# Kernel tuning notes

Hardware: AMD Instinct MI355X
Metric: run time of the kernel (lower is better)

Reference implementation:

```python
import jax, jax.numpy as jnp
import numpy as np

N = 500000       # total points
V = 60000        # number of voxels (segments)
XYZ_NORM = jnp.array([20.0, 20.0, 4.0], dtype=jnp.float32)
LN_EPS = 1e-3


def _ln(x, g, b):
    m = jnp.mean(x, axis=-1, keepdims=True)
    v = jnp.var(x, axis=-1, keepdims=True)
    return (x - m) * jax.lax.rsqrt(v + LN_EPS) * g + b


def _mlp_layer(x, w, b, g, be):
    # Linear -> LayerNorm -> ReLU (build_mlp in SST)
    return jax.nn.relu(_ln(x @ w + b, g, be))


def setup_inputs() -> dict:
    key = jax.random.key(0)
    ks = jax.random.split(key, 16)
    d = {
        "points": jax.random.normal(ks[0], (N, 4), jnp.float32) * 10.0,
        "features": jax.random.normal(ks[1], (N, 125), jnp.float32),
        "coors": jax.random.randint(ks[2], (N,), 0, V, jnp.int32),
        "f_cluster": jax.random.normal(ks[3], (N, 3), jnp.float32),
        "w1": jax.random.normal(ks[4], (128, 128), jnp.float32) * 0.05,
        "b1": jnp.zeros((128,), jnp.float32),
        "g1": jnp.ones((128,), jnp.float32),
        "be1": jnp.zeros((128,), jnp.float32),
        "w2": jax.random.normal(ks[5], (128, 256), jnp.float32) * 0.05,
        "b2": jnp.zeros((256,), jnp.float32),
        "g2": jnp.ones((256,), jnp.float32),
        "be2": jnp.zeros((256,), jnp.float32),
        "pw1": jax.random.normal(ks[6], (256, 256), jnp.float32) * 0.05,
        "pb1": jnp.zeros((256,), jnp.float32),
        "pg1": jnp.ones((256,), jnp.float32),
        "pbe1": jnp.zeros((256,), jnp.float32),
        "pw2": jax.random.normal(ks[7], (256, 256), jnp.float32) * 0.05,
        "pb2": jnp.zeros((256,), jnp.float32),
        "pg2": jnp.ones((256,), jnp.float32),
        "pbe2": jnp.zeros((256,), jnp.float32),
        "ow": jax.random.normal(ks[8], (256, 64), jnp.float32) * 0.05,
        "ob": jnp.zeros((64,), jnp.float32),
        "og": jnp.ones((64,), jnp.float32),
        "obe": jnp.zeros((64,), jnp.float32),
    }
    return d


def reference(points, features, coors, f_cluster,
              w1, b1, g1, be1, w2, b2, g2, be2,
              pw1, pb1, pg1, pbe1, pw2, pb2, pg2, pbe2,
              ow, ob, og, obe):
    fc = f_cluster / XYZ_NORM[None, :]
    x = jnp.concatenate([features, fc], axis=1)           # [N, 128]
    x = _mlp_layer(x, w1, b1, g1, be1)                     # [N, 128]
    x = _mlp_layer(x, w2, b2, g2, be2)                     # [N, 256]

    out_pts_feats = _mlp_layer(x, ow, ob, og, obe)         # [N, 64]

    counts = jax.ops.segment_sum(jnp.ones((x.shape[0],), x.dtype), coors,
                                 num_segments=V)           # [V]
    occ = counts > 0

    # scatter max aggregation
    agg = jax.ops.segment_max(x, coors, num_segments=V)    # [V, 256]
    agg = jnp.where(occ[:, None], agg, 0.0)
    agg = _mlp_layer(agg, pw1, pb1, pg1, pbe1)
    agg_feats = _mlp_layer(agg, pw2, pb2, pg2, pbe2)       # [V, 256]

    # scatter avg of xyz (computed in the original, used for out_coors path)
    xyz_sum = jax.ops.segment_sum(points[:, :3], coors, num_segments=V)
    cluster_xyz = xyz_sum / jnp.maximum(counts, 1.0)[:, None]
    out_coors = jnp.arange(V, dtype=jnp.int32)             # unique voxel ids
    del cluster_xyz  # not returned by the original forward

    return (out_pts_feats, agg_feats, out_coors)
```

## Files before the change

kernel.cpp:

```cpp
#include <hip/hip_runtime.h>


typedef __attribute__((ext_vector_type(4))) float f32x4;
typedef __attribute__((ext_vector_type(8))) short s16x8;
typedef __attribute__((ext_vector_type(2))) unsigned int u32x2;
typedef __attribute__((ext_vector_type(4))) unsigned int u32x4;

static constexpr int NP = 500000;
static constexpr int NV = 60000;

__device__ __forceinline__ unsigned short f2bf(float f){
  unsigned int u = __float_as_uint(f);
  u = (u + 0x7FFFu + ((u >> 16) & 1u)) >> 16;
  return (unsigned short)u;
}

__device__ __forceinline__ unsigned int cvtpk(float lo, float hi){
  unsigned int r;
  asm("v_cvt_pk_bf16_f32 %0, %1, %2" : "=v"(r) : "v"(lo), "v"(hi));
  return r;
}

__device__ __forceinline__ unsigned int pkmaxu16(unsigned int a, unsigned int b){
  unsigned int r;
  asm("v_pk_max_u16 %0, %1, %2" : "=v"(r) : "v"(a), "v"(b));
  return r;
}

__device__ __forceinline__ void pack_one(const float* __restrict__ w,
                                         unsigned short* __restrict__ dst,
                                         int K, int C, bool perm, int idx){
  int j = idx & 7, l = (idx >> 3) & 63, rest = idx >> 9;
  int kcn = K >> 5;
  int kc = rest % kcn, n = rest / kcn;
  int g = l >> 4, t = l & 15;
  int k = perm ? (kc * 32 + ((j >> 2) << 4) + g * 4 + (j & 3))
               : (kc * 32 + g * 8 + j);
  dst[idx] = f2bf(w[(size_t)k * C + n * 16 + t]);
}

__global__ void pack_hist_kernel(const float* __restrict__ w1, const float* __restrict__ w2,
                                 const float* __restrict__ ow, const float* __restrict__ pw1,
                                 const float* __restrict__ pw2,
                                 unsigned short* __restrict__ w1p, unsigned short* __restrict__ w2p,
                                 unsigned short* __restrict__ owp, unsigned short* __restrict__ pw1p,
                                 unsigned short* __restrict__ pw2p,
                                 float* __restrict__ out_coors,
                                 const int* __restrict__ coors, int* __restrict__ counts){
  int stride = gridDim.x * blockDim.x;
  const int T = 196608 + NV + NP;
  for (int i = blockIdx.x * blockDim.x + threadIdx.x; i < T; i += stride){
    if      (i < 16384)       pack_one(w1,  w1p,  128, 128, false, i);
    else if (i < 49152)       pack_one(w2,  w2p,  128, 256, true,  i - 16384);
    else if (i < 65536)       pack_one(ow,  owp,  256, 64,  true,  i - 49152);
    else if (i < 131072)      pack_one(pw1, pw1p, 256, 256, true,  i - 65536);
    else if (i < 196608)      pack_one(pw2, pw2p, 256, 256, true,  i - 131072);
    else if (i < 196608 + NV) out_coors[i - 196608] = (float)(i - 196608);
    else                      atomicAdd(&counts[coors[i - 196608 - NV]], 1);
  }
}

__global__ __launch_bounds__(1024)
void scan_kernel(const int* __restrict__ counts, int* __restrict__ cursor){
  __shared__ int part[1024];
  const int t = threadIdx.x;
  constexpr int PER = (NV + 1023) / 1024;
  int s = 0;
  for (int i = 0; i < PER; ++i){ int v = i * 1024 + t; if (v < NV) s += counts[v]; }
  part[t] = s;
  __syncthreads();
  for (int d = 1; d < 1024; d <<= 1){
    int u = (t >= d) ? part[t - d] : 0;
    __syncthreads();
    part[t] += u;
    __syncthreads();
  }
  int run = (t > 0) ? part[t - 1] : 0;
  for (int i = 0; i < PER; ++i){
    int v = i * 1024 + t;
    if (v < NV){ cursor[v] = run; run += counts[v]; }
  }
}

__global__ void scatter_prep2_kernel(const int* __restrict__ coors, int* __restrict__ cursor,
                                     const float* __restrict__ feats,
                                     const float* __restrict__ fclus,
                                     int2* __restrict__ pv,
                                     unsigned int* __restrict__ x0u){
  const int lane = threadIdx.x & 63;
  const int wid  = (blockIdx.x * blockDim.x + threadIdx.x) >> 6;
  const int nw   = (gridDim.x * blockDim.x) >> 6;
  const int NB = NP >> 6;
  const int c0 = 2 * lane, c1 = c0 + 1;
  const float s0 = (c0 >= 125) ? ((c0 == 127) ? 0.25f : 0.05f) : 1.f;
  const float s1 = (c1 >= 125) ? ((c1 == 127) ? 0.25f : 0.05f) : 1.f;

  for (int b = wid; b <= NB; b += nw){
    if (b < NB){
      const int i = b * 64 + lane;
      int v = coors[i];
      int p = atomicAdd(&cursor[v], 1);
      pv[p] = make_int2(i, v);
#pragma unroll 8
      for (int j = 0; j < 64; ++j){
        const int ij = b * 64 + j;
        const int pj = __shfl(p, j);
        const float* rp = feats + (size_t)ij * 125;
        const float* fc = fclus + (size_t)ij * 3;
        float v0 = (c0 < 125) ? rp[c0] : fc[c0 - 125];
        float v1 = (c1 < 125) ? rp[c1] : fc[c1 - 125];
        x0u[(size_t)pj * 64 + lane] = cvtpk(v0 * s0, v1 * s1);
      }
    } else {
      const int i = b * 64 + lane;
      int p = 0;
      if (lane < 32){
        int v = coors[i];
        p = atomicAdd(&cursor[v], 1);
        pv[p] = make_int2(i, v);
      }
#pragma unroll 8
      for (int j = 0; j < 32; ++j){
        const int ij = b * 64 + j;
        const int pj = __shfl(p, j);
        const float* rp = feats + (size_t)ij * 125;
        const float* fc = fclus + (size_t)ij * 3;
        float v0 = (c0 < 125) ? rp[c0] : fc[c0 - 125];
        float v1 = (c1 < 125) ? rp[c1] : fc[c1 - 125];
        x0u[(size_t)pj * 64 + lane] = cvtpk(v0 * s0, v1 * s1);
      }
    }
  }
}

template<int KC, int NT>
__device__ __forceinline__ void gemm2x(const s16x8* bA, const s16x8* bB,
                                       const unsigned short* __restrict__ Wp,
                                       int lane, f32x4* dA, f32x4* dB){
#pragma unroll
  for (int n = 0; n < NT; ++n){
    f32x4 aA = {0.f,0.f,0.f,0.f}, aB = {0.f,0.f,0.f,0.f};
#pragma unroll
    for (int kc = 0; kc < KC; ++kc){
      s16x8 w = *(const s16x8*)(Wp + ((n * KC + kc) * 64 + lane) * 8);
      aA = __builtin_amdgcn_mfma_f32_16x16x32_bf16(w, bA[kc], aA, 0, 0, 0);
      aB = __builtin_amdgcn_mfma_f32_16x16x32_bf16(w, bB[kc], aB, 0, 0, 0);
    }
    dA[n] = aA; dB[n] = aB;
  }
}

template<int NT, int C>
__device__ __forceinline__ void bias_ln_relu_sw(f32x4* d0, f32x4* d1,
                                                const float* __restrict__ bias,
                                                const float* __restrict__ gam,
                                                const float* __restrict__ bet, int g){
  float s0 = 0.f, s1 = 0.f, q0 = 0.f, q1 = 0.f;
#pragma unroll
  for (int n = 0; n < NT; ++n){
    f32x4 bv = *(const f32x4*)(bias + n * 16 + g * 4);
#pragma unroll
    for (int i = 0; i < 4; ++i){
      float v0 = d0[n][i] + bv[i]; d0[n][i] = v0; s0 += v0; q0 += v0 * v0;
      float v1 = d1[n][i] + bv[i]; d1[n][i] = v1; s1 += v1; q1 += v1 * v1;
    }
  }
  s0 += __shfl_xor(s0, 16); s0 += __shfl_xor(s0, 32);
  q0 += __shfl_xor(q0, 16); q0 += __shfl_xor(q0, 32);
  s1 += __shfl_xor(s1, 16); s1 += __shfl_xor(s1, 32);
  q1 += __shfl_xor(q1, 16); q1 += __shfl_xor(q1, 32);
  float m0 = s0 * (1.f / C), m1 = s1 * (1.f / C);
  float r0 = rsqrtf(q0 * (1.f / C) - m0 * m0 + 1e-3f);
  float r1 = rsqrtf(q1 * (1.f / C) - m1 * m1 + 1e-3f);
#pragma unroll
  for (int n = 0; n < NT; ++n){
    f32x4 gv  = *(const f32x4*)(gam + n * 16 + g * 4);
    f32x4 bev = *(const f32x4*)(bet + n * 16 + g * 4);
#pragma unroll
    for (int i = 0; i < 4; ++i){
      d0[n][i] = fmaxf((d0[n][i] - m0) * r0 * gv[i] + bev[i], 0.f);
      d1[n][i] = fmaxf((d1[n][i] - m1) * r1 * gv[i] + bev[i], 0.f);
    }
  }
}

template<int NT>
__device__ __forceinline__ void to_frags(const f32x4* d, s16x8* f){
#pragma unroll
  for (int kc = 0; kc < NT / 2; ++kc){
    u32x4 t;
    t[0] = cvtpk(d[2*kc][0],   d[2*kc][1]);
    t[1] = cvtpk(d[2*kc][2],   d[2*kc][3]);
    t[2] = cvtpk(d[2*kc+1][0], d[2*kc+1][1]);
    t[3] = cvtpk(d[2*kc+1][2], d[2*kc+1][3]);
    f[kc] = __builtin_bit_cast(s16x8, t);
  }
}

__device__ __forceinline__ void flush4(float* __restrict__ agg, int v, int lane,
                                       unsigned int q0, unsigned int q1, bool partial){
  float* base = agg + (size_t)v * 256 + lane * 4;
  unsigned int a0 = q0 << 16, a1 = q0 & 0xffff0000u;
  unsigned int a2 = q1 << 16, a3 = q1 & 0xffff0000u;
  if (!partial){
    f32x4 o;
    o[0] = __uint_as_float(a0); o[1] = __uint_as_float(a1);
    o[2] = __uint_as_float(a2); o[3] = __uint_as_float(a3);
    *(f32x4*)base = o;
  } else {
    unsigned int* ab = (unsigned int*)base;
    atomicMax(ab + 0, a0); atomicMax(ab + 1, a1);
    atomicMax(ab + 2, a2); atomicMax(ab + 3, a3);
  }
}

__global__ __launch_bounds__(256, 2)
void point_fused_kernel(const unsigned short* __restrict__ x0,
                        const int2* __restrict__ pv,
                        const unsigned short* __restrict__ w1p,
                        const unsigned short* __restrict__ w2p,
                        const unsigned short* __restrict__ owp,
                        const float* __restrict__ b1, const float* __restrict__ g1,
                        const float* __restrict__ be1,
                        const float* __restrict__ b2, const float* __restrict__ g2,
                        const float* __restrict__ be2,
                        const float* __restrict__ ob, const float* __restrict__ og,
                        const float* __restrict__ obe,
                        float* __restrict__ agg,
                        float* __restrict__ out_pts){
  __shared__ __align__(16) unsigned short tile[4][32 * 256];
  const int lane = threadIdx.x & 63;
  const int wave = threadIdx.x >> 6;
  const int g = lane >> 4, t = lane & 15;
  const int m0 = blockIdx.x * 128 + wave * 32;
  if (m0 >= NP) return;
  const int slotA = m0 + t, slotB = m0 + 16 + t;
  const int2 pA = pv[slotA];
  const int2 pB = pv[slotB];
  const int origA = pA.x, origB = pB.x;
  const int myv = pv[m0 + (lane & 31)].y;

  s16x8 bfA[4], bfB[4];
#pragma unroll
  for (int kc = 0; kc < 4; ++kc){
    bfA[kc] = *(const s16x8*)(x0 + (size_t)slotA * 128 + (kc * 4 + g) * 8);
    bfB[kc] = *(const s16x8*)(x0 + (size_t)slotB * 128 + (kc * 4 + g) * 8);
  }

  f32x4 d1a[8], d1b[8];
  gemm2x<4, 8>(bfA, bfB, w1p, lane, d1a, d1b);
  bias_ln_relu_sw<8, 128>(d1a, d1b, b1, g1, be1, g);
  s16x8 f2a[4], f2b[4];
  to_frags<8>(d1a, f2a); to_frags<8>(d1b, f2b);

  f32x4 d2a[16], d2b[16];
  gemm2x<4, 16>(f2a, f2b, w2p, lane, d2a, d2b);
  bias_ln_relu_sw<16, 256>(d2a, d2b, b2, g2, be2, g);
  s16x8 f3a[8], f3b[8];
  to_frags<16>(d2a, f3a); to_frags<16>(d2b, f3b);

  unsigned short* my = tile[wave];
  const int rA = t, rB = t + 16;
#pragma unroll
  for (int kc = 0; kc < 8; ++kc){
    int s = kc * 4 + g;
    int spA = (s & ~7) | ((s & 7) ^ (rA & 7));
    int spB = (s & ~7) | ((s & 7) ^ (rB & 7));
    *(s16x8*)&my[rA * 256 + spA * 8] = f3a[kc];
    *(s16x8*)&my[rB * 256 + spB * 8] = f3b[kc];
  }

  {
    f32x4 d3a[4], d3b[4];
    gemm2x<8, 4>(f3a, f3b, owp, lane, d3a, d3b);
    bias_ln_relu_sw<4, 64>(d3a, d3b, ob, og, obe, g);
#pragma unroll
    for (int n = 0; n < 4; ++n){
      *(f32x4*)(out_pts + (size_t)origA * 64 + n * 16 + g * 4) = d3a[n];
      *(f32x4*)(out_pts + (size_t)origB * 64 + n * 16 + g * 4) = d3b[n];
    }
  }

  const int vleft  = (m0 > 0) ? pv[m0 - 1].y : -1;
  const int vright = (m0 + 32 < NP) ? pv[m0 + 32].y : -1;
  const int slot = lane >> 1;
  const int half = (lane & 1) * 4;
  unsigned int q0 = 0, q1 = 0;
  int cur = __shfl(myv, 0);
  int rs = 0;
#pragma unroll
  for (int rc = 0; rc < 4; ++rc){
    u32x2 dreg[8];
#pragma unroll
    for (int rr = 0; rr < 8; ++rr){
      int r = rc * 8 + rr;
      int sp = (slot & ~7) | ((slot & 7) ^ (r & 7));
      dreg[rr] = *(const u32x2*)&my[r * 256 + sp * 8 + half];
    }
#pragma unroll
    for (int rr = 0; rr < 8; ++rr){
      int r = rc * 8 + rr;
      int v = __shfl(myv, r);
      if (v != cur){
        flush4(agg, cur, lane, q0, q1, rs == 0 && cur == vleft);
        q0 = 0; q1 = 0; cur = v; rs = r;
      }
      q0 = pkmaxu16(q0, dreg[rr][0]);
      q1 = pkmaxu16(q1, dreg[rr][1]);
    }
  }
  flush4(agg, cur, lane, q0, q1, (rs == 0 && cur == vleft) || cur == vright);
}

__global__ __launch_bounds__(256, 2)
void vox_fused_kernel(const float* __restrict__ agg,
                      const unsigned short* __restrict__ pw1p,
                      const unsigned short* __restrict__ pw2p,
                      const float* __restrict__ pb1, const float* __restrict__ pg1,
                      const float* __restrict__ pbe1,
                      const float* __restrict__ pb2, const float* __restrict__ pg2,
                      const float* __restrict__ pbe2,
                      float* __restrict__ out_vox){
  const int lane = threadIdx.x & 63;
  const int wave = threadIdx.x >> 6;
  const int m0 = blockIdx.x * 128 + wave * 32;
  if (m0 >= NV) return;
  const int g = lane >> 4, t = lane & 15;
  const size_t mA = m0 + t, mB = m0 + 16 + t;

  s16x8 bfA[8], bfB[8];
#pragma unroll
  for (int kc = 0; kc < 8; ++kc){
    const float* pa = agg + mA * 256 + kc * 32 + g * 8;
    const float* pb = agg + mB * 256 + kc * 32 + g * 8;
    f32x4 a0 = *(const f32x4*)pa, a1 = *(const f32x4*)(pa + 4);
    f32x4 b0 = *(const f32x4*)pb, b1v = *(const f32x4*)(pb + 4);
    u32x4 ta, tb;
    ta[0] = cvtpk(a0[0], a0[1]); ta[1] = cvtpk(a0[2], a0[3]);
    ta[2] = cvtpk(a1[0], a1[1]); ta[3] = cvtpk(a1[2], a1[3]);
    tb[0] = cvtpk(b0[0], b0[1]); tb[1] = cvtpk(b0[2], b0[3]);
    tb[2] = cvtpk(b1v[0], b1v[1]); tb[3] = cvtpk(b1v[2], b1v[3]);
    bfA[kc] = __builtin_bit_cast(s16x8, ta);
    bfB[kc] = __builtin_bit_cast(s16x8, tb);
  }
  f32x4 da[16], db[16];
  gemm2x<8, 16>(bfA, bfB, pw1p, lane, da, db);
  bias_ln_relu_sw<16, 256>(da, db, pb1, pg1, pbe1, g);

  s16x8 fa[8], fb[8];
  to_frags<16>(da, fa); to_frags<16>(db, fb);

  gemm2x<8, 16>(fa, fb, pw2p, lane, da, db);
  bias_ln_relu_sw<16, 256>(da, db, pb2, pg2, pbe2, g);
#pragma unroll
  for (int n = 0; n < 16; ++n){
    *(f32x4*)(out_vox + mA * 256 + n * 16 + g * 4) = da[n];
    *(f32x4*)(out_vox + mB * 256 + n * 16 + g * 4) = db[n];
  }
}

extern "C" void kernel_launch(void* const* d_in, const int* in_sizes, int n_in,
                              void* d_out, int out_size, void* d_ws, size_t ws_size,
                              hipStream_t stream){
  const float* features  = (const float*)d_in[1];
  const int*   coors     = (const int*)  d_in[2];
  const float* f_cluster = (const float*)d_in[3];
  const float* w1  = (const float*)d_in[4];
  const float* b1  = (const float*)d_in[5];
  const float* g1  = (const float*)d_in[6];
  const float* be1 = (const float*)d_in[7];
  const float* w2  = (const float*)d_in[8];
  const float* b2  = (const float*)d_in[9];
  const float* g2  = (const float*)d_in[10];
  const float* be2 = (const float*)d_in[11];
  const float* pw1 = (const float*)d_in[12];
  const float* pb1 = (const float*)d_in[13];
  const float* pg1 = (const float*)d_in[14];
  const float* pbe1= (const float*)d_in[15];
  const float* pw2 = (const float*)d_in[16];
  const float* pb2 = (const float*)d_in[17];
  const float* pg2 = (const float*)d_in[18];
  const float* pbe2= (const float*)d_in[19];
  const float* ow  = (const float*)d_in[20];
  const float* ob  = (const float*)d_in[21];
  const float* og  = (const float*)d_in[22];
  const float* obe = (const float*)d_in[23];

  char* ws = (char*)d_ws;
  float* aggf   = (float*)(ws + 0);
  int* counts   = (int*)(ws + 61440000ull);
  int* cursor   = (int*)(ws + 61800000ull);
  int2* pv      = (int2*)(ws + 62100000ull);
  unsigned int* x0u = (unsigned int*)(ws + 66200000ull);
  unsigned short* x0 = (unsigned short*)x0u;
  unsigned short* w1p = (unsigned short*)(ws + 195000000ull);
  unsigned short* w2p = (unsigned short*)(ws + 195000000ull + 1*262144ull);
  unsigned short* owp = (unsigned short*)(ws + 195000000ull + 2*262144ull);
  unsigned short* pw1p= (unsigned short*)(ws + 195000000ull + 3*262144ull);
  unsigned short* pw2p= (unsigned short*)(ws + 195000000ull + 4*262144ull);

  float* outp      = (float*)d_out;
  float* out_pts   = outp;
  float* out_vox   = outp + 32000000;
  float* out_coors = outp + 47360000;

  hipMemsetAsync(ws, 0, 61440000ull + (size_t)NV * sizeof(int), stream);

  pack_hist_kernel<<<2048, 256, 0, stream>>>(w1, w2, ow, pw1, pw2,
                                             w1p, w2p, owp, pw1p, pw2p,
                                             out_coors, coors, counts);

  scan_kernel<<<1, 1024, 0, stream>>>(counts, cursor);

  scatter_prep2_kernel<<<2048, 256, 0, stream>>>(coors, cursor, features, f_cluster,
                                                 pv, x0u);

  point_fused_kernel<<<(NP + 127) / 128, 256, 0, stream>>>(
      x0, pv, w1p, w2p, owp,
      b1, g1, be1, b2, g2, be2, ob, og, obe, aggf, out_pts);

  vox_fused_kernel<<<(NV + 127) / 128, 256, 0, stream>>>(
      aggf, pw1p, pw2p, pb1, pg1, pbe1, pb2, pg2, pbe2, out_vox);
}
```

Before: 549.6 us.

## Process 16 points per wave in point kernel to raise occupancy

Each wave in the fused point MLP kernel now handles one 16-row MFMA tile instead of two. This roughly halves accumulator register and LDS tile usage, and launch bounds are raised to allow four blocks per CU. The goal is more concurrent waves to hide memory latency in the gather, scatter and max-aggregation phases. In exchange, each weight fragment loaded feeds only one MFMA instead of two, so weight traffic per point doubles. The change also adds s_setprio around the GEMMs and unrolls the scan loops.

Measured after the change: 654.3 us. 19.1% more time.

```diff
diff --git a/kernel.cpp b/kernel.cpp
--- a/kernel.cpp
+++ b/kernel.cpp
@@ -66,6 +66,7 @@
   const int t = threadIdx.x;
   constexpr int PER = (NV + 1023) / 1024;
   int s = 0;
+#pragma unroll
   for (int i = 0; i < PER; ++i){ int v = i * 1024 + t; if (v < NV) s += counts[v]; }
   part[t] = s;
   __syncthreads();
@@ -76,6 +77,7 @@
     __syncthreads();
   }
   int run = (t > 0) ? part[t - 1] : 0;
+#pragma unroll
   for (int i = 0; i < PER; ++i){
     int v = i * 1024 + t;
     if (v < NV){ cursor[v] = run; run += counts[v]; }
@@ -134,6 +136,63 @@
 }
 
 template<int KC, int NT>
+__device__ __forceinline__ void gemm1x(const s16x8* bf,
+                                       const unsigned short* __restrict__ Wp,
+                                       int lane, f32x4* d){
+#pragma unroll
+  for (int n = 0; n < NT; ++n){
+    f32x4 a = {0.f,0.f,0.f,0.f};
+#pragma unroll
+    for (int kc = 0; kc < KC; ++kc){
+      s16x8 w = *(const s16x8*)(Wp + ((n * KC + kc) * 64 + lane) * 8);
+      a = __builtin_amdgcn_mfma_f32_16x16x32_bf16(w, bf[kc], a, 0, 0, 0);
+    }
+    d[n] = a;
+  }
+}
+
+template<int NT, int C>
+__device__ __forceinline__ void bias_ln_relu_1(f32x4* d,
+                                               const float* __restrict__ bias,
+                                               const float* __restrict__ gam,
+                                               const float* __restrict__ bet, int g){
+  float s = 0.f, q = 0.f;
+#pragma unroll
+  for (int n = 0; n < NT; ++n){
+    f32x4 bv = *(const f32x4*)(bias + n * 16 + g * 4);
+#pragma unroll
+    for (int i = 0; i < 4; ++i){
+      float v = d[n][i] + bv[i]; d[n][i] = v; s += v; q += v * v;
+    }
+  }
+  s += __shfl_xor(s, 16); s += __shfl_xor(s, 32);
+  q += __shfl_xor(q, 16); q += __shfl_xor(q, 32);
+  float m = s * (1.f / C);
+  float r = rsqrtf(q * (1.f / C) - m * m + 1e-3f);
+#pragma unroll
+  for (int n = 0; n < NT; ++n){
+    f32x4 gv  = *(const f32x4*)(gam + n * 16 + g * 4);
+    f32x4 bev = *(const f32x4*)(bet + n * 16 + g * 4);
+#pragma unroll
+    for (int i = 0; i < 4; ++i)
+      d[n][i] = fmaxf((d[n][i] - m) * r * gv[i] + bev[i], 0.f);
+  }
+}
+
+template<int NT>
+__device__ __forceinline__ void to_frags1(const f32x4* d, s16x8* f){
+#pragma unroll
+  for (int kc = 0; kc < NT / 2; ++kc){
+    u32x4 t;
+    t[0] = cvtpk(d[2*kc][0],   d[2*kc][1]);
+    t[1] = cvtpk(d[2*kc][2],   d[2*kc][3]);
+    t[2] = cvtpk(d[2*kc+1][0], d[2*kc+1][1]);
+    t[3] = cvtpk(d[2*kc+1][2], d[2*kc+1][3]);
+    f[kc] = __builtin_bit_cast(s16x8, t);
+  }
+}
+
+template<int KC, int NT>
 __device__ __forceinline__ void gemm2x(const s16x8* bA, const s16x8* bB,
                                        const unsigned short* __restrict__ Wp,
                                        int lane, f32x4* dA, f32x4* dB){
@@ -214,7 +273,7 @@
   }
 }
 
-__global__ __launch_bounds__(256, 2)
+__global__ __launch_bounds__(256, 4)
 void point_fused_kernel(const unsigned short* __restrict__ x0,
                         const int2* __restrict__ pv,
                         const unsigned short* __restrict__ w1p,
@@ -228,68 +287,66 @@
                         const float* __restrict__ obe,
                         float* __restrict__ agg,
                         float* __restrict__ out_pts){
-  __shared__ __align__(16) unsigned short tile[4][32 * 256];
+  __shared__ __align__(16) unsigned short tile[4][16 * 256];
   const int lane = threadIdx.x & 63;
   const int wave = threadIdx.x >> 6;
   const int g = lane >> 4, t = lane & 15;
-  const int m0 = blockIdx.x * 128 + wave * 32;
+  const int m0 = blockIdx.x * 64 + wave * 16;
   if (m0 >= NP) return;
-  const int slotA = m0 + t, slotB = m0 + 16 + t;
-  const int2 pA = pv[slotA];
-  const int2 pB = pv[slotB];
-  const int origA = pA.x, origB = pB.x;
-  const int myv = pv[m0 + (lane & 31)].y;
-
-  s16x8 bfA[4], bfB[4];
-#pragma unroll
-  for (int kc = 0; kc < 4; ++kc){
-    bfA[kc] = *(const s16x8*)(x0 + (size_t)slotA * 128 + (kc * 4 + g) * 8);
-    bfB[kc] = *(const s16x8*)(x0 + (size_t)slotB * 128 + (kc * 4 + g) * 8);
-  }
-
-  f32x4 d1a[8], d1b[8];
-  gemm2x<4, 8>(bfA, bfB, w1p, lane, d1a, d1b);
-  bias_ln_relu_sw<8, 128>(d1a, d1b, b1, g1, be1, g);
-  s16x8 f2a[4], f2b[4];
-  to_frags<8>(d1a, f2a); to_frags<8>(d1b, f2b);
-
-  f32x4 d2a[16], d2b[16];
-  gemm2x<4, 16>(f2a, f2b, w2p, lane, d2a, d2b);
-  bias_ln_relu_sw<16, 256>(d2a, d2b, b2, g2, be2, g);
-  s16x8 f3a[8], f3b[8];
-  to_frags<16>(d2a, f3a); to_frags<16>(d2b, f3b);
+  const int slot0 = m0 + t;
+  const int2 p0 = pv[slot0];
+  const int orig = p0.x;
+  const int myv = pv[m0 + (lane & 15)].y;
+
+  s16x8 bf[4];
+#pragma unroll
+  for (int kc = 0; kc < 4; ++kc)
+    bf[kc] = *(const s16x8*)(x0 + (size_t)slot0 * 128 + (kc * 4 + g) * 8);
+
+  f32x4 d1[8];
+  __builtin_amdgcn_s_setprio(1);
+  gemm1x<4, 8>(bf, w1p, lane, d1);
+  __builtin_amdgcn_s_setprio(0);
+  bias_ln_relu_1<8, 128>(d1, b1, g1, be1, g);
+  s16x8 f2[4];
+  to_frags1<8>(d1, f2);
+
+  f32x4 d2[16];
+  __builtin_amdgcn_s_setprio(1);
+  gemm1x<4, 16>(f2, w2p, lane, d2);
+  __builtin_amdgcn_s_setprio(0);
+  bias_ln_relu_1<16, 256>(d2, b2, g2, be2, g);
+  s16x8 f3[8];
+  to_frags1<16>(d2, f3);
 
   unsigned short* my = tile[wave];
-  const int rA = t, rB = t + 16;
 #pragma unroll
   for (int kc = 0; kc < 8; ++kc){
     int s = kc * 4 + g;
-    int spA = (s & ~7) | ((s & 7) ^ (rA & 7));
-    int spB = (s & ~7) | ((s & 7) ^ (rB & 7));
-    *(s16x8*)&my[rA * 256 + spA * 8] = f3a[kc];
-    *(s16x8*)&my[rB * 256 + spB * 8] = f3b[kc];
+    int sp = (s & ~7) | ((s & 7) ^ (t & 7));
+    *(s16x8*)&my[t * 256 + sp * 8] = f3[kc];
   }
 
   {
-    f32x4 d3a[4], d3b[4];
-    gemm2x<8, 4>(f3a, f3b, owp, lane, d3a, d3b);
-    bias_ln_relu_sw<4, 64>(d3a, d3b, ob, og, obe, g);
-#pragma unroll
-    for (int n = 0; n < 4; ++n){
-      *(f32x4*)(out_pts + (size_t)origA * 64 + n * 16 + g * 4) = d3a[n];
-      *(f32x4*)(out_pts + (size_t)origB * 64 + n * 16 + g * 4) = d3b[n];
-    }
+    f32x4 d3[4];
+    __builtin_amdgcn_s_setprio(1);
+    gemm1x<8, 4>(f3, owp, lane, d3);
+    __builtin_amdgcn_s_setprio(0);
+    bias_ln_relu_1<4, 64>(d3, ob, og, obe, g);
+#pragma unroll
+    for (int n = 0; n < 4; ++n)
+      *(f32x4*)(out_pts + (size_t)orig * 64 + n * 16 + g * 4) = d3[n];
   }
 
   const int vleft  = (m0 > 0) ? pv[m0 - 1].y : -1;
-  const int vright = (m0 + 32 < NP) ? pv[m0 + 32].y : -1;
+  const int vright = (m0 + 16 < NP) ? pv[m0 + 16].y : -1;
   const int slot = lane >> 1;
   const int half = (lane & 1) * 4;
   unsigned int q0 = 0, q1 = 0;
   int cur = __shfl(myv, 0);
   int rs = 0;
 #pragma unroll
-  for (int rc = 0; rc < 4; ++rc){
+  for (int rc = 0; rc < 2; ++rc){
     u32x2 dreg[8];
 #pragma unroll
     for (int rr = 0; rr < 8; ++rr){
@@ -415,7 +472,7 @@
   scatter_prep2_kernel<<<2048, 256, 0, stream>>>(coors, cursor, features, f_cluster,
                                                  pv, x0u);
 
-  point_fused_kernel<<<(NP + 127) / 128, 256, 0, stream>>>(
+  point_fused_kernel<<<(NP + 63) / 64, 256, 0, stream>>>(
       x0, pv, w1p, w2p, owp,
       b1, g1, be1, b2, g2, be2, ob, og, obe, aggf, out_pts);
 
```

## Halve point kernel LDS tile and raise occupancy to three blocks per CU

Applied to the files above, without the earlier changes.

The per-wave LDS staging tile for the segment-max reduction shrinks from 32 rows to 16. The two 16-row halves are now written and reduced one after the other, with a scheduling barrier between them. Launch bounds go from 2 to 3 blocks per CU so that more waves can hide memory latency. The scan kernel loops are also unrolled. The extra occupancy target tightens the register budget and could cause spills in this large fused GEMM kernel.

New measurement: 685.7 us. 24.8% more time.

```diff
diff --git a/kernel.cpp b/kernel.cpp
--- a/kernel.cpp
+++ b/kernel.cpp
@@ -66,6 +66,7 @@
   const int t = threadIdx.x;
   constexpr int PER = (NV + 1023) / 1024;
   int s = 0;
+#pragma unroll
   for (int i = 0; i < PER; ++i){ int v = i * 1024 + t; if (v < NV) s += counts[v]; }
   part[t] = s;
   __syncthreads();
@@ -76,6 +77,7 @@
     __syncthreads();
   }
   int run = (t > 0) ? part[t - 1] : 0;
+#pragma unroll
   for (int i = 0; i < PER; ++i){
     int v = i * 1024 + t;
     if (v < NV){ cursor[v] = run; run += counts[v]; }
@@ -214,7 +216,7 @@
   }
 }
 
-__global__ __launch_bounds__(256, 2)
+__global__ __launch_bounds__(256, 3)
 void point_fused_kernel(const unsigned short* __restrict__ x0,
                         const int2* __restrict__ pv,
                         const unsigned short* __restrict__ w1p,
@@ -228,7 +230,7 @@
                         const float* __restrict__ obe,
                         float* __restrict__ agg,
                         float* __restrict__ out_pts){
-  __shared__ __align__(16) unsigned short tile[4][32 * 256];
+  __shared__ __align__(16) unsigned short tile[4][16 * 256];
   const int lane = threadIdx.x & 63;
   const int wave = threadIdx.x >> 6;
   const int g = lane >> 4, t = lane & 15;
@@ -260,14 +262,11 @@
   to_frags<16>(d2a, f3a); to_frags<16>(d2b, f3b);
 
   unsigned short* my = tile[wave];
-  const int rA = t, rB = t + 16;
 #pragma unroll
   for (int kc = 0; kc < 8; ++kc){
     int s = kc * 4 + g;
-    int spA = (s & ~7) | ((s & 7) ^ (rA & 7));
-    int spB = (s & ~7) | ((s & 7) ^ (rB & 7));
-    *(s16x8*)&my[rA * 256 + spA * 8] = f3a[kc];
-    *(s16x8*)&my[rB * 256 + spB * 8] = f3b[kc];
+    int sp = (s & ~7) | ((s & 7) ^ (t & 7));
+    *(s16x8*)&my[t * 256 + sp * 8] = f3a[kc];
   }
 
   {
@@ -288,8 +287,9 @@
   unsigned int q0 = 0, q1 = 0;
   int cur = __shfl(myv, 0);
   int rs = 0;
-#pragma unroll
-  for (int rc = 0; rc < 4; ++rc){
+
+#pragma unroll
+  for (int rc = 0; rc < 2; ++rc){
     u32x2 dreg[8];
 #pragma unroll
     for (int rr = 0; rr < 8; ++rr){
@@ -304,6 +304,37 @@
       if (v != cur){
         flush4(agg, cur, lane, q0, q1, rs == 0 && cur == vleft);
         q0 = 0; q1 = 0; cur = v; rs = r;
+      }
+      q0 = pkmaxu16(q0, dreg[rr][0]);
+      q1 = pkmaxu16(q1, dreg[rr][1]);
+    }
+  }
+
+  __builtin_amdgcn_sched_barrier(0);
+
+#pragma unroll
+  for (int kc = 0; kc < 8; ++kc){
+    int s = kc * 4 + g;
+    int sp = (s & ~7) | ((s & 7) ^ (t & 7));
+    *(s16x8*)&my[t * 256 + sp * 8] = f3b[kc];
+  }
+
+#pragma unroll
+  for (int rc = 0; rc < 2; ++rc){
+    u32x2 dreg[8];
+#pragma unroll
+    for (int rr = 0; rr < 8; ++rr){
+      int r = rc * 8 + rr;
+      int sp = (slot & ~7) | ((slot & 7) ^ (r & 7));
+      dreg[rr] = *(const u32x2*)&my[r * 256 + sp * 8 + half];
+    }
+#pragma unroll
+    for (int rr = 0; rr < 8; ++rr){
+      int gr = 16 + rc * 8 + rr;
+      int v = __shfl(myv, gr);
+      if (v != cur){
+        flush4(agg, cur, lane, q0, q1, rs == 0 && cur == vleft);
+        q0 = 0; q1 = 0; cur = v; rs = gr;
       }
       q0 = pkmaxu16(q0, dreg[rr][0]);
       q1 = pkmaxu16(q1, dreg[rr][1]);
```
